# Kernel tuning notes

Measured on AMD Instinct MI355X. Metric: run time of the kernel, lower is better.

Reference implementation:

```python
import jax, jax.numpy as jnp
import numpy as np

D = 768
HID = 4 * D
B = 16
HRES = 32
WRES = 32
T = HRES * WRES


def layernorm(x, g, b, eps=1e-5):
    m = jnp.mean(x, axis=-1, keepdims=True)
    v = jnp.mean(jnp.square(x - m), axis=-1, keepdims=True)
    return (x - m) * jax.lax.rsqrt(v + eps) * g + b


def q_shift(x, H, W):
    # Vision-RWKV quad-directional token shift: split channels into 4 groups,
    # each group takes the neighboring patch's value in one direction (zero pad).
    Bn, N, C = x.shape
    xi = x.reshape(Bn, H, W, C)
    c = C // 4
    g0 = jnp.pad(xi[:, :, :-1, 0 * c:1 * c], ((0, 0), (0, 0), (1, 0), (0, 0)))  # from left
    g1 = jnp.pad(xi[:, :, 1:, 1 * c:2 * c], ((0, 0), (0, 0), (0, 1), (0, 0)))   # from right
    g2 = jnp.pad(xi[:, :-1, :, 2 * c:3 * c], ((0, 0), (1, 0), (0, 0), (0, 0)))  # from above
    g3 = jnp.pad(xi[:, 1:, :, 3 * c:4 * c], ((0, 0), (0, 1), (0, 0), (0, 0)))   # from below
    return jnp.concatenate([g0, g1, g2, g3], axis=-1).reshape(Bn, N, C)


def wkv_scan(w_log, u, k, v):
    # Numerically stable RWKV WKV recurrence (per-channel linear attention).
    # k, v: [B, T, C]; w = -exp(w_log) is the per-channel decay, u the bonus.
    w = -jnp.exp(w_log)
    kT = jnp.swapaxes(k, 0, 1)  # [T, B, C]
    vT = jnp.swapaxes(v, 0, 1)
    Bn, C = k.shape[0], k.shape[2]
    aa0 = jnp.zeros((Bn, C), k.dtype)
    bb0 = jnp.zeros((Bn, C), k.dtype)
    pp0 = jnp.full((Bn, C), -1e30, k.dtype)

    def step(carry, kv):
        aa, bb, pp = carry
        kt, vt = kv
        ww = u + kt
        p = jnp.maximum(pp, ww)
        e1 = jnp.exp(pp - p)
        e2 = jnp.exp(ww - p)
        out = (e1 * aa + e2 * vt) / (e1 * bb + e2)
        ww2 = pp + w
        p2 = jnp.maximum(ww2, kt)
        e1b = jnp.exp(ww2 - p2)
        e2b = jnp.exp(kt - p2)
        return (e1b * aa + e2b * vt, e1b * bb + e2b, p2), out

    _, outT = jax.lax.scan(step, (aa0, bb0, pp0), (kT, vT))
    return jnp.swapaxes(outT, 0, 1)  # [B, T, C]


def setup_inputs() -> dict:
    key = jax.random.key(0)
    ks = jax.random.split(key, 16)

    def nrm(k, shape, s=0.02):
        return jax.random.normal(k, shape, jnp.float32) * s

    return {
        "x": jax.random.normal(ks[0], (B, T, D), jnp.float32),
        "H": HRES,
        "W": WRES,
        "ln1_g": jnp.ones((D,), jnp.float32),
        "ln1_b": jnp.zeros((D,), jnp.float32),
        "ln2_g": jnp.ones((D,), jnp.float32),
        "ln2_b": jnp.zeros((D,), jnp.float32),
        "mu_k": jax.random.uniform(ks[1], (D,), jnp.float32),
        "mu_v": jax.random.uniform(ks[2], (D,), jnp.float32),
        "mu_r": jax.random.uniform(ks[3], (D,), jnp.float32),
        "w_log": nrm(ks[4], (D,), 0.5),
        "u": nrm(ks[5], (D,), 0.5),
        "Wk": nrm(ks[6], (D, D)),
        "Wv": nrm(ks[7], (D, D)),
        "Wr": nrm(ks[8], (D, D)),
        "Wo": nrm(ks[9], (D, D)),
        "cmu_k": jax.random.uniform(ks[10], (D,), jnp.float32),
        "cmu_r": jax.random.uniform(ks[11], (D,), jnp.float32),
        "Ck": nrm(ks[12], (HID, D)),
        "Cv": nrm(ks[13], (D, HID)),
        "Cr": nrm(ks[14], (D, D)),
    }


def reference(x, H, W, ln1_g, ln1_b, ln2_g, ln2_b, mu_k, mu_v, mu_r, w_log, u,
              Wk, Wv, Wr, Wo, cmu_k, cmu_r, Ck, Cv, Cr):
    h = x
    # ---- spatial mix (RWKV time-mix over patch sequence) ----
    a = layernorm(h, ln1_g, ln1_b)
    sx = q_shift(a, H, W)
    xk = a * mu_k + sx * (1.0 - mu_k)
    xv = a * mu_v + sx * (1.0 - mu_v)
    xr = a * mu_r + sx * (1.0 - mu_r)
    k = xk @ Wk.T
    v = xv @ Wv.T
    r = jax.nn.sigmoid(xr @ Wr.T)
    wkv = wkv_scan(w_log, u, k, v)
    h = h + (r * wkv) @ Wo.T
    # ---- channel mix (squared-ReLU gated FFN) ----
    a2 = layernorm(h, ln2_g, ln2_b)
    sx2 = q_shift(a2, H, W)
    xk2 = a2 * cmu_k + sx2 * (1.0 - cmu_k)
    xr2 = a2 * cmu_r + sx2 * (1.0 - cmu_r)
    kk = jnp.square(jax.nn.relu(xk2 @ Ck.T))
    h = h + jax.nn.sigmoid(xr2 @ Cr.T) * (kk @ Cv.T)
    # ---- outer residual from RWKVBlock.forward ----
    return h + x
```

## Files before the change

### kernel.cpp

```cpp
#include <hip/hip_runtime.h>
#include <hip/hip_bf16.h>

#define DD   768
#define TT   1024
#define BBATCH 16
#define NROWS (BBATCH * TT)
#define HIDN 3072
#define HHALF 1536
#define HH 32
#define WW 32
#define DW  (DD * DD)
#define DH  (DD * HIDN)
#define CCH 64
#define PCH (TT / CCH)

typedef float  floatx4 __attribute__((ext_vector_type(4)));
typedef __bf16 bf16x8  __attribute__((ext_vector_type(8)));

__device__ __forceinline__ float bf2f(__hip_bfloat16 v) { return __bfloat162float(v); }
__device__ __forceinline__ __hip_bfloat16 f2bf(float v) { return __float2bfloat16(v); }
__device__ __forceinline__ float toF(__hip_bfloat16 v) { return __bfloat162float(v); }
__device__ __forceinline__ float toF(float v) { return v; }

__device__ __forceinline__ void load4f(const float* __restrict__ p, float o[4]) {
    const float4 v = *reinterpret_cast<const float4*>(p);
    o[0] = v.x; o[1] = v.y; o[2] = v.z; o[3] = v.w;
}
__device__ __forceinline__ void load4f(const __hip_bfloat16* __restrict__ p, float o[4]) {
    const ushort4 v = *reinterpret_cast<const ushort4*>(p);
    o[0] = bf2f(__hip_bfloat16_raw{v.x});
    o[1] = bf2f(__hip_bfloat16_raw{v.y});
    o[2] = bf2f(__hip_bfloat16_raw{v.z});
    o[3] = bf2f(__hip_bfloat16_raw{v.w});
}
__device__ __forceinline__ void load8f(const float* __restrict__ p, float o[8]) {
    load4f(p, o); load4f(p + 4, o + 4);
}
__device__ __forceinline__ void load8f(const __hip_bfloat16* __restrict__ p, float o[8]) {
    const uint4 v = *reinterpret_cast<const uint4*>(p);
    const unsigned short* s = reinterpret_cast<const unsigned short*>(&v);
#pragma unroll
    for (int e = 0; e < 8; ++e) o[e] = bf2f(__hip_bfloat16_raw{s[e]});
}

#define GL2LDS(gp, lp)  __builtin_amdgcn_global_load_lds(                     \
    (const __attribute__((address_space(1))) void*)(gp),                      \
    (__attribute__((address_space(3))) void*)(lp), 16, 0, 0)

__global__ __launch_bounds__(256)
void cvt_all(const float* __restrict__ w0, const float* __restrict__ w1,
             const float* __restrict__ w2, const float* __restrict__ w3,
             const float* __restrict__ w4, const float* __restrict__ w5,
             const float* __restrict__ w6, __hip_bfloat16* __restrict__ dst)
{
    const int b = blockIdx.x;
    const float* s; size_t dofs; int rel;
    if (b < 2880) {
        const int seg = b / 576; rel = b - seg * 576;
        s = seg == 0 ? w0 : seg == 1 ? w1 : seg == 2 ? w2 : seg == 3 ? w3 : w4;
        dofs = (size_t)seg * DW;
    } else if (b < 5184) {
        rel = b - 2880; s = w5; dofs = 5ull * DW;
    } else {
        rel = b - 5184; s = w6; dofs = 5ull * DW + DH;
    }
    const int i = rel * 1024 + threadIdx.x * 4;
    const float4 v = *reinterpret_cast<const float4*>(s + i);
    __hip_bfloat16 o[4] = {f2bf(v.x), f2bf(v.y), f2bf(v.z), f2bf(v.w)};
    *reinterpret_cast<ushort4*>(&dst[dofs + i]) = *reinterpret_cast<const ushort4*>(o);
}

template <typename TIN>
__global__ __launch_bounds__(256)
void ln_stats_k(const TIN* __restrict__ x,
                float* __restrict__ mean, float* __restrict__ rstd)
{
    const int row  = blockIdx.x * 4 + (threadIdx.x >> 6);
    const int lane = threadIdx.x & 63;
    const TIN* xr = x + (size_t)row * DD;
    float s1 = 0.f, s2 = 0.f;
#pragma unroll
    for (int q = 0; q < 3; ++q) {
        float v4[4];
        load4f(xr + 4 * lane + 256 * q, v4);
#pragma unroll
        for (int e = 0; e < 4; ++e) { s1 += v4[e]; s2 += v4[e] * v4[e]; }
    }
#pragma unroll
    for (int off = 32; off > 0; off >>= 1) {
        s1 += __shfl_down(s1, off);
        s2 += __shfl_down(s2, off);
    }
    if (lane == 0) {
        const float m = s1 * (1.f / DD);
        mean[row] = m;
        rstd[row] = rsqrtf(s2 * (1.f / DD) - m * m + 1e-5f);
    }
}

template <typename TIN, int NOUT>
__global__ __launch_bounds__(256)
void mix_k(const TIN* __restrict__ x,
           const float* __restrict__ mean, const float* __restrict__ rstd,
           const float* __restrict__ g, const float* __restrict__ b,
           const float* __restrict__ muk,
           const float* __restrict__ muv,
           const float* __restrict__ mur,
           __hip_bfloat16* __restrict__ xk,
           __hip_bfloat16* __restrict__ xv,
           __hip_bfloat16* __restrict__ xr)
{
    const size_t i8 = ((size_t)blockIdx.x * 256 + threadIdx.x) * 8;
    const int c  = (int)(i8 % DD);
    const int n  = (int)((i8 / DD) % TT);
    const int bb = (int)(i8 / ((size_t)DD * TT));
    const int y = n >> 5, xp = n & 31;
    const int grow = bb * TT + n;

    const int grp = c / (DD / 4);
    int ny = y, nx = xp; bool ok;
    if      (grp == 0) { nx = xp - 1; ok = xp > 0;      }
    else if (grp == 1) { nx = xp + 1; ok = xp < WW - 1; }
    else if (grp == 2) { ny = y - 1;  ok = y > 0;       }
    else               { ny = y + 1;  ok = y < HH - 1;  }

    float gg[8], bbv[8];
    load8f(g + c, gg); load8f(b + c, bbv);

    float xc[8];
    load8f(x + (size_t)grow * DD + c, xc);
    const float m = mean[grow], rs = rstd[grow];
    float av[8], sx[8] = {0.f, 0.f, 0.f, 0.f, 0.f, 0.f, 0.f, 0.f};
#pragma unroll
    for (int e = 0; e < 8; ++e) av[e] = (xc[e] - m) * rs * gg[e] + bbv[e];

    if (ok) {
        const int nrow = bb * TT + ny * WW + nx;
        float xn[8];
        load8f(x + (size_t)nrow * DD + c, xn);
        const float m2 = mean[nrow], rs2 = rstd[nrow];
#pragma unroll
        for (int e = 0; e < 8; ++e) sx[e] = (xn[e] - m2) * rs2 * gg[e] + bbv[e];
    }

    float mk[8], mr[8];
    load8f(muk + c, mk); load8f(mur + c, mr);
    __hip_bfloat16 ok8[8], or8[8];
#pragma unroll
    for (int e = 0; e < 8; ++e) {
        ok8[e] = f2bf(av[e] * mk[e] + sx[e] * (1.f - mk[e]));
        or8[e] = f2bf(av[e] * mr[e] + sx[e] * (1.f - mr[e]));
    }
    *reinterpret_cast<uint4*>(&xk[i8]) = *reinterpret_cast<const uint4*>(ok8);
    *reinterpret_cast<uint4*>(&xr[i8]) = *reinterpret_cast<const uint4*>(or8);
    if (NOUT == 3) {
        float mv[8];
        load8f(muv + c, mv);
        __hip_bfloat16 ov8[8];
#pragma unroll
        for (int e = 0; e < 8; ++e)
            ov8[e] = f2bf(av[e] * mv[e] + sx[e] * (1.f - mv[e]));
        *reinterpret_cast<uint4*>(&xv[i8]) = *reinterpret_cast<const uint4*>(ov8);
    }
}

__device__ __forceinline__ void xpose_band(const floatx4 accRow[4], float* scr,
                                           int lane, float cv[16])
{
    const int l15 = lane & 15, quad = lane >> 4;
#pragma unroll
    for (int j = 0; j < 4; ++j)
#pragma unroll
        for (int r = 0; r < 4; ++r)
            scr[(quad * 4 + r) * 68 + j * 16 + l15] = accRow[j][r];
    const int row_l = lane >> 2, cb = (lane & 3) * 16;
#pragma unroll
    for (int q = 0; q < 4; ++q)
        *reinterpret_cast<float4*>(&cv[q * 4]) =
            *reinterpret_cast<const float4*>(&scr[row_l * 68 + cb + q * 4]);
}

template <int MODE>
__device__ __forceinline__ void mode_store(
    const float cv[16], size_t idx,
    __hip_bfloat16* __restrict__ outB, float* __restrict__ outF,
    const __hip_bfloat16* __restrict__ auxS, const __hip_bfloat16* __restrict__ auxH,
    const float* __restrict__ auxX, const float* __restrict__ auxG)
{
    if (MODE == 1 || MODE == 3) {
        __hip_bfloat16 ob[16];
#pragma unroll
        for (int e = 0; e < 16; ++e) {
            float v = cv[e];
            if (MODE == 1) v = 1.f / (1.f + __expf(-v));
            else { v = fmaxf(v, 0.f); v = v * v; }
            ob[e] = f2bf(v);
        }
        *reinterpret_cast<uint4*>(&outB[idx])     = *reinterpret_cast<const uint4*>(&ob[0]);
        *reinterpret_cast<uint4*>(&outB[idx + 8]) = *reinterpret_cast<const uint4*>(&ob[8]);
    } else if (MODE == 2) {
        float xv[16];
#pragma unroll
        for (int q = 0; q < 4; ++q)
            *reinterpret_cast<float4*>(&xv[q * 4]) =
                *reinterpret_cast<const float4*>(&auxX[idx + q * 4]);
        __hip_bfloat16 ob[16];
#pragma unroll
        for (int e = 0; e < 16; ++e) ob[e] = f2bf(cv[e] + xv[e]);
        *reinterpret_cast<uint4*>(&outB[idx])     = *reinterpret_cast<const uint4*>(&ob[0]);
        *reinterpret_cast<uint4*>(&outB[idx + 8]) = *reinterpret_cast<const uint4*>(&ob[8]);
    } else if (MODE == 4) {
        unsigned short hs[16], ss[16]; float xv[16], ov[16];
        *reinterpret_cast<uint4*>(&hs[0]) = *reinterpret_cast<const uint4*>(&auxH[idx]);
        *reinterpret_cast<uint4*>(&hs[8]) = *reinterpret_cast<const uint4*>(&auxH[idx + 8]);
        *reinterpret_cast<uint4*>(&ss[0]) = *reinterpret_cast<const uint4*>(&auxS[idx]);
        *reinterpret_cast<uint4*>(&ss[8]) = *reinterpret_cast<const uint4*>(&auxS[idx + 8]);
#pragma unroll
        for (int q = 0; q < 4; ++q)
            *reinterpret_cast<float4*>(&xv[q * 4]) =
                *reinterpret_cast<const float4*>(&auxX[idx + q * 4]);
#pragma unroll
        for (int e = 0; e < 16; ++e)
            ov[e] = bf2f(__hip_bfloat16_raw{hs[e]})
                  + bf2f(__hip_bfloat16_raw{ss[e]}) * cv[e] + xv[e];
#pragma unroll
        for (int q = 0; q < 4; ++q)
            *reinterpret_cast<float4*>(&outF[idx + q * 4]) =
                *reinterpret_cast<const float4*>(&ov[q * 4]);
    } else if (MODE == 5) {
        unsigned short ss[16]; float ov[16];
        *reinterpret_cast<uint4*>(&ss[0]) = *reinterpret_cast<const uint4*>(&auxS[idx]);
        *reinterpret_cast<uint4*>(&ss[8]) = *reinterpret_cast<const uint4*>(&auxS[idx + 8]);
#pragma unroll
        for (int q = 0; q < 4; ++q)
            *reinterpret_cast<float4*>(&ov[q * 4]) =
                *reinterpret_cast<const float4*>(&outF[idx + q * 4]);
#pragma unroll
        for (int e = 0; e < 16; ++e)
            ov[e] += bf2f(__hip_bfloat16_raw{ss[e]}) * cv[e];
#pragma unroll
        for (int q = 0; q < 4; ++q)
            *reinterpret_cast<float4*>(&outF[idx + q * 4]) =
                *reinterpret_cast<const float4*>(&ov[q * 4]);
    } else if (MODE == 6) {
        unsigned short hs[16]; float xv[16], gf[16], ov[16];
        *reinterpret_cast<uint4*>(&hs[0]) = *reinterpret_cast<const uint4*>(&auxH[idx]);
        *reinterpret_cast<uint4*>(&hs[8]) = *reinterpret_cast<const uint4*>(&auxH[idx + 8]);
#pragma unroll
        for (int q = 0; q < 4; ++q) {
            *reinterpret_cast<float4*>(&xv[q * 4]) =
                *reinterpret_cast<const float4*>(&auxX[idx + q * 4]);
            *reinterpret_cast<float4*>(&gf[q * 4]) =
                *reinterpret_cast<const float4*>(&auxG[idx + q * 4]);
        }
#pragma unroll
        for (int e = 0; e < 16; ++e)
            ov[e] = bf2f(__hip_bfloat16_raw{hs[e]}) + gf[e] * cv[e] + xv[e];
#pragma unroll
        for (int q = 0; q < 4; ++q)
            *reinterpret_cast<float4*>(&outF[idx + q * 4]) =
                *reinterpret_cast<const float4*>(&ov[q * 4]);
    } else {
        float ov[16];
#pragma unroll
        for (int e = 0; e < 16; ++e)
            ov[e] = 1.f / (1.f + __expf(-cv[e]));
#pragma unroll
        for (int q = 0; q < 4; ++q)
            *reinterpret_cast<float4*>(&outF[idx + q * 4]) =
                *reinterpret_cast<const float4*>(&ov[q * 4]);
    }
}

#define BM 128
#define BN 128
#define BKK 64

__device__ __forceinline__ void gemm_core(
    const __hip_bfloat16* __restrict__ A, const __hip_bfloat16* __restrict__ W,
    int K, int Wstr, int bm, int bn, unsigned short* lds, floatx4 acc[4][4])
{
    const int tid  = threadIdx.x;
    const int lane = tid & 63, wid = tid >> 6;
    const int l15  = lane & 15, quad = lane >> 4;
    const int m0   = (wid & 1) * 64;
    const int n0   = (wid >> 1) * 64;
    const int srow  = lane >> 3;
    const int gcolg = (lane & 7) ^ srow;
    const int s0    = wid * 4;
    const int swzbase = l15 & 7;

    for (int k0 = 0; k0 < K; k0 += BKK) {
#pragma unroll
        for (int t = 0; t < 4; ++t) {
            const int s   = s0 + t;
            const int row = s * 8 + srow;
            GL2LDS(A + (size_t)(bm * BM + row) * K    + k0 + gcolg * 8,
                   &lds[s * 512]);
            GL2LDS(W + (size_t)(bn * BN + row) * Wstr + k0 + gcolg * 8,
                   &lds[8192 + s * 512]);
        }
        __syncthreads();
#pragma unroll
        for (int kk = 0; kk < BKK; kk += 32) {
            const int swz = (((kk >> 3) + quad) ^ swzbase) * 8;
            bf16x8 afr[4], bfr[4];
#pragma unroll
            for (int i = 0; i < 4; ++i)
                afr[i] = *reinterpret_cast<const bf16x8*>(
                    &lds[(m0 + i * 16 + l15) * BKK + swz]);
#pragma unroll
            for (int j = 0; j < 4; ++j)
                bfr[j] = *reinterpret_cast<const bf16x8*>(
                    &lds[8192 + (n0 + j * 16 + l15) * BKK + swz]);
#pragma unroll
            for (int i = 0; i < 4; ++i)
#pragma unroll
                for (int j = 0; j < 4; ++j)
                    acc[i][j] = __builtin_amdgcn_mfma_f32_16x16x32_bf16(
                        afr[i], bfr[j], acc[i][j], 0, 0, 0);
        }
        __syncthreads();
    }
}

template <int MODE>
__global__ __launch_bounds__(256, 2)
void gemm_bt(const __hip_bfloat16* __restrict__ A,
             const __hip_bfloat16* __restrict__ W,
             int K, int Wstr, int Nn,
             __hip_bfloat16* __restrict__ outB,
             float* __restrict__ outF,
             const __hip_bfloat16* __restrict__ auxS,
             const __hip_bfloat16* __restrict__ auxH,
             const float* __restrict__ auxX,
             const float* __restrict__ auxG)
{
    __shared__ __align__(16) unsigned short lds[16384];
    const int bm = blockIdx.x, bn = blockIdx.y;
    const int tid = threadIdx.x, lane = tid & 63, wid = tid >> 6;
    const int m0 = (wid & 1) * 64, n0 = (wid >> 1) * 64;

    floatx4 acc[4][4];
#pragma unroll
    for (int i = 0; i < 4; ++i)
#pragma unroll
        for (int j = 0; j < 4; ++j)
            acc[i][j] = floatx4{0.f, 0.f, 0.f, 0.f};

    gemm_core(A, W, K, Wstr, bm, bn, lds, acc);

    float* scr = reinterpret_cast<float*>(lds) + wid * 1088;
    const int row_l = lane >> 2, cb = (lane & 3) * 16;
#pragma unroll
    for (int i = 0; i < 4; ++i) {
        float cv[16];
        xpose_band(acc[i], scr, lane, cv);
        const int grow = bm * BM + m0 + i * 16 + row_l;
        const int gcol = bn * BN + n0 + cb;
        const size_t idx = (size_t)grow * Nn + gcol;
        mode_store<MODE>(cv, idx, outB, outF, auxS, auxH, auxX, auxG);
    }
}

__global__ __launch_bounds__(256, 2)
void gemm_qkv(const __hip_bfloat16* __restrict__ A0, const __hip_bfloat16* __restrict__ A1,
              const __hip_bfloat16* __restrict__ A2,
              const __hip_bfloat16* __restrict__ W0, const __hip_bfloat16* __restrict__ W1,
              const __hip_bfloat16* __restrict__ W2,
              __hip_bfloat16* __restrict__ O0, __hip_bfloat16* __restrict__ O1,
              __hip_bfloat16* __restrict__ O2)
{
    __shared__ __align__(16) unsigned short lds[16384];
    const int z = blockIdx.z;
    const __hip_bfloat16* A = z == 0 ? A0 : z == 1 ? A1 : A2;
    const __hip_bfloat16* W = z == 0 ? W0 : z == 1 ? W1 : W2;
    __hip_bfloat16*       O = z == 0 ? O0 : z == 1 ? O1 : O2;
    const int bm = blockIdx.x, bn = blockIdx.y;
    const int tid = threadIdx.x, lane = tid & 63, wid = tid >> 6;
    const int m0 = (wid & 1) * 64, n0 = (wid >> 1) * 64;

    floatx4 acc[4][4];
#pragma unroll
    for (int i = 0; i < 4; ++i)
#pragma unroll
        for (int j = 0; j < 4; ++j)
            acc[i][j] = floatx4{0.f, 0.f, 0.f, 0.f};

    gemm_core(A, W, DD, DD, bm, bn, lds, acc);

    float* scr = reinterpret_cast<float*>(lds) + wid * 1088;
    const int row_l = lane >> 2, cb = (lane & 3) * 16;
#pragma unroll
    for (int i = 0; i < 4; ++i) {
        float cv[16];
        xpose_band(acc[i], scr, lane, cv);
        const int grow = bm * BM + m0 + i * 16 + row_l;
        const int gcol = bn * BN + n0 + cb;
        const size_t idx = (size_t)grow * DD + gcol;
        __hip_bfloat16 ob[16];
#pragma unroll
        for (int e = 0; e < 16; ++e) {
            float v = cv[e];
            if (z == 2) v = 1.f / (1.f + __expf(-v));
            ob[e] = f2bf(v);
        }
        *reinterpret_cast<uint4*>(&O[idx])     = *reinterpret_cast<const uint4*>(&ob[0]);
        *reinterpret_cast<uint4*>(&O[idx + 8]) = *reinterpret_cast<const uint4*>(&ob[8]);
    }
}

__global__ __launch_bounds__(192)
void wkv_passA(const float* __restrict__ w_log,
               const __hip_bfloat16* __restrict__ k,
               const __hip_bfloat16* __restrict__ v,
               float* __restrict__ SA, float* __restrict__ SB,
               float* __restrict__ SP)
{
    const int c  = threadIdx.x * 4;
    const int j  = blockIdx.x;
    const int bb = blockIdx.y;
    float wl[4];
    load4f(w_log + c, wl);
    const float w4[4] = {-__expf(wl[0]), -__expf(wl[1]), -__expf(wl[2]), -__expf(wl[3])};
    const size_t base = ((size_t)bb * TT + j * CCH) * DD + c;
    float a[4] = {0.f, 0.f, 0.f, 0.f}, b2[4] = {0.f, 0.f, 0.f, 0.f};
    float p[4] = {-1e30f, -1e30f, -1e30f, -1e30f};
#pragma unroll 4
    for (int t = 0; t < CCH; ++t) {
        const size_t o = base + (size_t)t * DD;
        float kt[4], vt[4];
        load4f(k + o, kt);
        load4f(v + o, vt);
#pragma unroll
        for (int e = 0; e < 4; ++e) {
            const float ww2 = p[e] + w4[e];
            const float p2  = fmaxf(ww2, kt[e]);
            const float e1  = __expf(ww2 - p2);
            const float e2  = __expf(kt[e] - p2);
            a[e]  = e1 * a[e]  + e2 * vt[e];
            b2[e] = e1 * b2[e] + e2;
            p[e]  = p2;
        }
    }
    const size_t si = ((size_t)bb * PCH + j) * DD + c;
    *reinterpret_cast<float4*>(&SA[si]) = float4{a[0], a[1], a[2], a[3]};
    *reinterpret_cast<float4*>(&SB[si]) = float4{b2[0], b2[1], b2[2], b2[3]};
    *reinterpret_cast<float4*>(&SP[si]) = float4{p[0], p[1], p[2], p[3]};
}

__global__ __launch_bounds__(256)
void wkv_scanj(const float* __restrict__ w_log,
               float* __restrict__ SA, float* __restrict__ SB,
               float* __restrict__ SP)
{
    const int idx = blockIdx.x * 256 + threadIdx.x;
    const int c = (idx * 4) % DD, bb = (idx * 4) / DD;
    float wl[4];
    load4f(w_log + c, wl);
    float wC[4];
#pragma unroll
    for (int e = 0; e < 4; ++e) wC[e] = -__expf(wl[e]) * (float)CCH;
    float a[4] = {0.f, 0.f, 0.f, 0.f}, b2[4] = {0.f, 0.f, 0.f, 0.f};
    float p[4] = {-1e30f, -1e30f, -1e30f, -1e30f};
#pragma unroll
    for (int j = 0; j < PCH; ++j) {
        const size_t si = ((size_t)bb * PCH + j) * DD + c;
        float aj[4], bj[4], pj[4];
        load4f(SA + si, aj); load4f(SB + si, bj); load4f(SP + si, pj);
        *reinterpret_cast<float4*>(&SA[si]) = float4{a[0], a[1], a[2], a[3]};
        *reinterpret_cast<float4*>(&SB[si]) = float4{b2[0], b2[1], b2[2], b2[3]};
        *reinterpret_cast<float4*>(&SP[si]) = float4{p[0], p[1], p[2], p[3]};
#pragma unroll
        for (int e = 0; e < 4; ++e) {
            const float pd = p[e] + wC[e];
            const float pn = fmaxf(pd, pj[e]);
            const float e1 = __expf(pd - pn);
            const float e2 = __expf(pj[e] - pn);
            a[e]  = e1 * a[e]  + e2 * aj[e];
            b2[e] = e1 * b2[e] + e2 * bj[e];
            p[e]  = pn;
        }
    }
}

__global__ __launch_bounds__(192)
void wkv_passB(const float* __restrict__ w_log, const float* __restrict__ u,
               const __hip_bfloat16* __restrict__ k,
               const __hip_bfloat16* __restrict__ v,
               const __hip_bfloat16* __restrict__ r,
               __hip_bfloat16* __restrict__ rw,
               const float* __restrict__ SA, const float* __restrict__ SB,
               const float* __restrict__ SP)
{
    const int c  = threadIdx.x * 4;
    const int j  = blockIdx.x;
    const int bb = blockIdx.y;
    float wl[4], uu[4];
    load4f(w_log + c, wl);
    load4f(u + c, uu);
    const float w4[4] = {-__expf(wl[0]), -__expf(wl[1]), -__expf(wl[2]), -__expf(wl[3])};
    const size_t si = ((size_t)bb * PCH + j) * DD + c;
    float aa[4], bbv[4], pp[4];
    load4f(SA + si, aa); load4f(SB + si, bbv); load4f(SP + si, pp);
    const size_t base = ((size_t)bb * TT + j * CCH) * DD + c;
#pragma unroll 4
    for (int t = 0; t < CCH; ++t) {
        const size_t o = base + (size_t)t * DD;
        float kt[4], vt[4], rt[4];
        load4f(k + o, kt);
        load4f(v + o, vt);
        load4f(r + o, rt);
        __hip_bfloat16 ob[4];
#pragma unroll
        for (int e = 0; e < 4; ++e) {
            const float ww = uu[e] + kt[e];
            const float pm = fmaxf(pp[e], ww);
            const float e1 = __expf(pp[e] - pm);
            const float e2 = __expf(ww - pm);
            const float ov = __fdividef(e1 * aa[e] + e2 * vt[e], e1 * bbv[e] + e2);
            ob[e] = f2bf(rt[e] * ov);
            const float ww2 = pp[e] + w4[e];
            const float p2  = fmaxf(ww2, kt[e]);
            const float e1b = __expf(ww2 - p2);
            const float e2b = __expf(kt[e] - p2);
            aa[e]  = e1b * aa[e]  + e2b * vt[e];
            bbv[e] = e1b * bbv[e] + e2b;
            pp[e]  = p2;
        }
        *reinterpret_cast<ushort4*>(&rw[o]) = *reinterpret_cast<const ushort4*>(ob);
    }
}

extern "C" void kernel_launch(void* const* d_in, const int* in_sizes, int n_in,
                              void* d_out, int out_size, void* d_ws, size_t ws_size,
                              hipStream_t stream)
{
    (void)in_sizes; (void)n_in; (void)out_size;
    const float* x     = (const float*)d_in[0];
    const float* ln1_g = (const float*)d_in[3];
    const float* ln1_b = (const float*)d_in[4];
    const float* ln2_g = (const float*)d_in[5];
    const float* ln2_b = (const float*)d_in[6];
    const float* mu_k  = (const float*)d_in[7];
    const float* mu_v  = (const float*)d_in[8];
    const float* mu_r  = (const float*)d_in[9];
    const float* w_log = (const float*)d_in[10];
    const float* u     = (const float*)d_in[11];
    const float* Wk    = (const float*)d_in[12];
    const float* Wv    = (const float*)d_in[13];
    const float* Wr    = (const float*)d_in[14];
    const float* Wo    = (const float*)d_in[15];
    const float* cmu_k = (const float*)d_in[16];
    const float* cmu_r = (const float*)d_in[17];
    const float* Ck    = (const float*)d_in[18];
    const float* Cv    = (const float*)d_in[19];
    const float* Cr    = (const float*)d_in[20];
    float* out = (float*)d_out;

    const size_t ND = (size_t)NROWS * DD;
    const size_t SL = ND * 2;
    const size_t WBYTES = (size_t)(5 * DW + 2 * DH) * 2;
    const size_t NSTATE = (size_t)BBATCH * PCH * DD;
    const size_t TAIL = WBYTES + 2 * (size_t)NROWS * sizeof(float)
                      + 3 * NSTATE * sizeof(float);
    int nslots;
    if      (ws_size >= 7 * SL + TAIL) nslots = 7;
    else if (ws_size >= 6 * SL + TAIL) nslots = 6;
    else if (ws_size >= 5 * SL + TAIL) nslots = 5;
    else return;

    char* w = (char*)d_ws;
    __hip_bfloat16* S0 = (__hip_bfloat16*)(w);
    __hip_bfloat16* S1 = (__hip_bfloat16*)(w + 1 * SL);
    __hip_bfloat16* S2 = (__hip_bfloat16*)(w + 2 * SL);
    __hip_bfloat16* S3 = (__hip_bfloat16*)(w + 3 * SL);
    __hip_bfloat16* S4 = (__hip_bfloat16*)(w + 4 * SL);
    __hip_bfloat16* S5 = (__hip_bfloat16*)(w + 5 * SL);
    __hip_bfloat16* WB  = (__hip_bfloat16*)(w + (size_t)nslots * SL);
    __hip_bfloat16* WkB = WB;
    __hip_bfloat16* WvB = WB + 1ull * DW;
    __hip_bfloat16* WrB = WB + 2ull * DW;
    __hip_bfloat16* WoB = WB + 3ull * DW;
    __hip_bfloat16* CrB = WB + 4ull * DW;
    __hip_bfloat16* CkB = WB + 5ull * DW;
    __hip_bfloat16* CvB = CkB + DH;
    float* meanB = (float*)(w + (size_t)nslots * SL + WBYTES);
    float* rstdB = meanB + NROWS;
    float* SAb = rstdB + NROWS;
    float* SBb = SAb + NSTATE;
    float* SPb = SBb + NSTATE;

    const int LN_GRID  = NROWS / 4;
    const int MIX_GRID = (int)(ND / 2048);
    const dim3 g768(NROWS / BM, DD / BN);
    const dim3 g1536(NROWS / BM, HHALF / BN);
    const dim3 gCk(NROWS / BM, HIDN / BN);
    const dim3 gqkv3(NROWS / BM, DD / BN, 3);
    const dim3 gqkv2(NROWS / BM, DD / BN, 2);
    const dim3 gwkv(PCH, BBATCH);
    const int SCANJ_GRID = (BBATCH * DD / 4) / 256;

    cvt_all<<<7488, 256, 0, stream>>>(Wk, Wv, Wr, Wo, Cr, Ck, Cv, WB);

    ln_stats_k<float><<<LN_GRID, 256, 0, stream>>>(x, meanB, rstdB);
    mix_k<float, 3><<<MIX_GRID, 256, 0, stream>>>(x, meanB, rstdB, ln1_g, ln1_b,
                                                  mu_k, mu_v, mu_r, S0, S1, S2);

    if (nslots == 7) {
        gemm_qkv<<<gqkv3, 256, 0, stream>>>(S0, S1, S2, WkB, WvB, WrB, S3, S4, S5);
        wkv_passA<<<gwkv, 192, 0, stream>>>(w_log, S3, S4, SAb, SBb, SPb);
        wkv_scanj<<<SCANJ_GRID, 256, 0, stream>>>(w_log, SAb, SBb, SPb);
        wkv_passB<<<gwkv, 192, 0, stream>>>(w_log, u, S3, S4, S5, S1, SAb, SBb, SPb);
        gemm_bt<2><<<g768, 256, 0, stream>>>(S1, WoB, DD, DD, DD, S2, nullptr,
                                             nullptr, nullptr, x, nullptr);
        ln_stats_k<__hip_bfloat16><<<LN_GRID, 256, 0, stream>>>(S2, meanB, rstdB);
        mix_k<__hip_bfloat16, 2><<<MIX_GRID, 256, 0, stream>>>(S2, meanB, rstdB, ln2_g, ln2_b,
                                                               cmu_k, nullptr, cmu_r,
                                                               S0, nullptr, S3);
        gemm_bt<1><<<g768, 256, 0, stream>>>(S3, CrB, DD, DD, DD, S1, nullptr,
                                             nullptr, nullptr, nullptr, nullptr);
        gemm_bt<3><<<gCk, 256, 0, stream>>>(S0, CkB, DD, DD, HIDN,
                                            S3, nullptr, nullptr, nullptr, nullptr, nullptr);
        gemm_bt<4><<<g768, 256, 0, stream>>>(S3, CvB, HIDN, HIDN, DD,
                                             nullptr, out, S1, S2, x, nullptr);
    } else if (nslots == 6) {
        gemm_qkv<<<gqkv3, 256, 0, stream>>>(S0, S1, S2, WkB, WvB, WrB, S3, S4, S5);
        wkv_passA<<<gwkv, 192, 0, stream>>>(w_log, S3, S4, SAb, SBb, SPb);
        wkv_scanj<<<SCANJ_GRID, 256, 0, stream>>>(w_log, SAb, SBb, SPb);
        wkv_passB<<<gwkv, 192, 0, stream>>>(w_log, u, S3, S4, S5, S0, SAb, SBb, SPb);
        gemm_bt<2><<<g768, 256, 0, stream>>>(S0, WoB, DD, DD, DD, S1, nullptr,
                                             nullptr, nullptr, x, nullptr);
        ln_stats_k<__hip_bfloat16><<<LN_GRID, 256, 0, stream>>>(S1, meanB, rstdB);
        mix_k<__hip_bfloat16, 2><<<MIX_GRID, 256, 0, stream>>>(S1, meanB, rstdB, ln2_g, ln2_b,
                                                               cmu_k, nullptr, cmu_r,
                                                               S0, nullptr, S2);
        gemm_bt<7><<<g768, 256, 0, stream>>>(S2, CrB, DD, DD, DD, nullptr, out,
                                             nullptr, nullptr, nullptr, nullptr);
        gemm_bt<3><<<gCk, 256, 0, stream>>>(S0, CkB, DD, DD, HIDN,
                                            S2, nullptr, nullptr, nullptr, nullptr, nullptr);
        gemm_bt<6><<<g768, 256, 0, stream>>>(S2, CvB, HIDN, HIDN, DD,
                                             nullptr, out, nullptr, S1, x, out);
    } else {
        gemm_qkv<<<gqkv2, 256, 0, stream>>>(S0, S1, nullptr, WkB, WvB, nullptr,
                                            S3, S4, nullptr);
        gemm_bt<1><<<g768, 256, 0, stream>>>(S2, WrB, DD, DD, DD, S0, nullptr,
                                             nullptr, nullptr, nullptr, nullptr);
        wkv_passA<<<gwkv, 192, 0, stream>>>(w_log, S3, S4, SAb, SBb, SPb);
        wkv_scanj<<<SCANJ_GRID, 256, 0, stream>>>(w_log, SAb, SBb, SPb);
        wkv_passB<<<gwkv, 192, 0, stream>>>(w_log, u, S3, S4, S0, S1, SAb, SBb, SPb);
        gemm_bt<2><<<g768, 256, 0, stream>>>(S1, WoB, DD, DD, DD, S2, nullptr,
                                             nullptr, nullptr, x, nullptr);
        ln_stats_k<__hip_bfloat16><<<LN_GRID, 256, 0, stream>>>(S2, meanB, rstdB);
        mix_k<__hip_bfloat16, 2><<<MIX_GRID, 256, 0, stream>>>(S2, meanB, rstdB, ln2_g, ln2_b,
                                                               cmu_k, nullptr, cmu_r,
                                                               S0, nullptr, S3);
        gemm_bt<1><<<g768, 256, 0, stream>>>(S3, CrB, DD, DD, DD, S1, nullptr,
                                             nullptr, nullptr, nullptr, nullptr);
        __hip_bfloat16* kk = S3;
        gemm_bt<3><<<g1536, 256, 0, stream>>>(S0, CkB, DD, DD, HHALF,
                                              kk, nullptr, nullptr, nullptr, nullptr, nullptr);
        gemm_bt<4><<<g768, 256, 0, stream>>>(kk, CvB, HHALF, HIDN, DD,
                                             nullptr, out, S1, S2, x, nullptr);
        gemm_bt<3><<<g1536, 256, 0, stream>>>(S0, CkB + (size_t)HHALF * DD, DD, DD, HHALF,
                                              kk, nullptr, nullptr, nullptr, nullptr, nullptr);
        gemm_bt<5><<<g768, 256, 0, stream>>>(kk, CvB + HHALF, HHALF, HIDN, DD,
                                             nullptr, out, S1, nullptr, nullptr, nullptr);
    }
}
```

Baseline: 540.5 us.

## Add 256x256-tile 8-wave pipelined GEMM for channel-mix Ck and Cv

Adds a new GEMM kernel with 256x256 output tiles, 512 threads and double-buffered global-to-LDS async loads interleaved with MFMA quarters under barriers and raised wave priority. It also adds a swizzled block-to-tile mapping. The kernel replaces the 128x128 GEMM for the two large channel-mix matmuls (Ck expansion and Cv projection). The goal is more operand reuse per loaded byte and better overlap of loads with MFMA. The cost is heavy register and LDS use (128KB LDS per block), fewer blocks per CU, and a possible wave-quantization tail on the smaller 768-wide grid.

```diff
diff --git a/kernel.cpp b/kernel.cpp
--- a/kernel.cpp
+++ b/kernel.cpp
@@ -47,6 +47,12 @@
     (const __attribute__((address_space(1))) void*)(gp),                      \
     (__attribute__((address_space(3))) void*)(lp), 16, 0, 0)
 
+#define BARX() __builtin_amdgcn_s_barrier()
+#define WAITV6() do { asm volatile("s_waitcnt vmcnt(6)");                      \
+    __builtin_amdgcn_sched_barrier(0); } while (0)
+#define WAITV0() do { asm volatile("s_waitcnt vmcnt(0)");                      \
+    __builtin_amdgcn_sched_barrier(0); } while (0)
+
 __global__ __launch_bounds__(256)
 void cvt_all(const float* __restrict__ w0, const float* __restrict__ w1,
              const float* __restrict__ w2, const float* __restrict__ w3,
@@ -269,6 +275,143 @@
         for (int q = 0; q < 4; ++q)
             *reinterpret_cast<float4*>(&outF[idx + q * 4]) =
                 *reinterpret_cast<const float4*>(&ov[q * 4]);
+    }
+}
+
+#define STG256(tau, j)                                                         \
+  do { if ((tau) * 64 < K) {                                                   \
+    const int _sb = ((((tau) & 1) * 4) + (j)) * 8192;                          \
+    const int _k0 = (tau) * 64;                                                \
+    const __hip_bfloat16 *_s0, *_s1;                                           \
+    if ((j) < 2) {                                                             \
+      _s0 = A + (size_t)(bmr + (j) * 128 + r0) * K + _k0 + colg;               \
+      _s1 = A + (size_t)(bmr + (j) * 128 + r1) * K + _k0 + colg;               \
+    } else {                                                                   \
+      const int _w0 = bnr + ((j) == 2 ? 128 : 0);                              \
+      _s0 = W + (size_t)(_w0 + r0) * Wstr + _k0 + colg;                        \
+      _s1 = W + (size_t)(_w0 + r1) * Wstr + _k0 + colg;                        \
+    }                                                                          \
+    GL2LDS(_s0, &lds[_sb + wid * 512]);                                        \
+    GL2LDS(_s1, &lds[_sb + 4096 + wid * 512]);                                 \
+  } } while (0)
+
+#define LDA_H(buf, mh)                                                         \
+  { const int _ab = ((buf) * 4 + wr) * 8192;                                   \
+    _Pragma("unroll") for (int mf = 0; mf < 4; ++mf)                           \
+    _Pragma("unroll") for (int k2 = 0; k2 < 2; ++k2)                           \
+      af[(mh) * 4 + mf][k2] = *reinterpret_cast<const bf16x8*>(                \
+        &lds[_ab + (((mh) * 4 + mf) * 16 + l15) * 64                           \
+             + (((k2 * 4 + quad) ^ sw7) * 8)]); }
+
+#define LDB_TO(dst, buf, nh)                                                   \
+  { const int _bb = ((buf) * 4 + ((wc >> 1) ? 2 : 3)) * 8192;                  \
+    _Pragma("unroll") for (int nf = 0; nf < 2; ++nf)                           \
+    _Pragma("unroll") for (int k2 = 0; k2 < 2; ++k2)                           \
+      dst[nf][k2] = *reinterpret_cast<const bf16x8*>(                          \
+        &lds[_bb + ((wc & 1) * 64 + (nh) * 32 + nf * 16 + l15) * 64            \
+             + (((k2 * 4 + quad) ^ sw7) * 8)]); }
+
+#define MFQ(MH, NH, BARR)                                                      \
+  _Pragma("unroll") for (int mf = 0; mf < 4; ++mf)                             \
+  _Pragma("unroll") for (int nf = 0; nf < 2; ++nf)                             \
+  _Pragma("unroll") for (int k2 = 0; k2 < 2; ++k2)                             \
+    acc[(MH) * 4 + mf][(NH) * 2 + nf] =                                        \
+      __builtin_amdgcn_mfma_f32_16x16x32_bf16(af[(MH) * 4 + mf][k2],           \
+        BARR[nf][k2], acc[(MH) * 4 + mf][(NH) * 2 + nf], 0, 0, 0);
+
+#define TILE_STEP(tt, buf)                                                     \
+  {                                                                            \
+    LDA_H(buf, 0); LDB_TO(bfa, buf, 0);                                        \
+    STG256((tt) + 1, 3);                                                       \
+    BARX();                                                                    \
+    __builtin_amdgcn_s_setprio(1); MFQ(0, 0, bfa); __builtin_amdgcn_s_setprio(0);\
+    BARX();                                                                    \
+    LDA_H(buf, 1);                                                             \
+    BARX();                                                                    \
+    __builtin_amdgcn_s_setprio(1); MFQ(1, 0, bfa); __builtin_amdgcn_s_setprio(0);\
+    BARX();                                                                    \
+    LDB_TO(bfb, buf, 1);                                                       \
+    STG256((tt) + 2, 0);                                                       \
+    BARX();                                                                    \
+    __builtin_amdgcn_s_setprio(1); MFQ(0, 1, bfb); __builtin_amdgcn_s_setprio(0);\
+    BARX();                                                                    \
+    STG256((tt) + 2, 1);                                                       \
+    STG256((tt) + 2, 2);                                                       \
+    BARX();                                                                    \
+    __builtin_amdgcn_s_setprio(1); MFQ(1, 1, bfb); __builtin_amdgcn_s_setprio(0);\
+    if ((tt) + 2 == nt) { WAITV0(); } else { WAITV6(); }                       \
+    BARX();                                                                    \
+  }
+
+struct G256Ctx {
+    int bm, bn;
+    int tid, lane, wid, wr, wc, l15, quad, sw7, r0, r1, colg;
+};
+
+__device__ __forceinline__ void g256_decode(G256Ctx& c, int b, int nbn, int nwg)
+{
+    const int s = (b & 7) * (nwg >> 3) + (b >> 3);
+    c.bm = s / nbn; c.bn = s % nbn;
+    c.tid = threadIdx.x; c.lane = c.tid & 63; c.wid = c.tid >> 6;
+    c.wr = c.wid >> 2; c.wc = c.wid & 3;
+    c.l15 = c.lane & 15; c.quad = c.lane >> 4; c.sw7 = c.l15 & 7;
+    c.r0 = c.tid >> 3; c.r1 = c.r0 + 64;
+    c.colg = ((c.tid & 7) ^ (c.r0 & 7)) * 8;
+}
+
+__device__ __forceinline__ void g256_core(
+    const __hip_bfloat16* __restrict__ A, const __hip_bfloat16* __restrict__ W,
+    int K, int Wstr, const G256Ctx& c, unsigned short* lds, floatx4 acc[8][4])
+{
+    const int bmr = c.bm * 256, bnr = c.bn * 256;
+    const int wid = c.wid, wr = c.wr, wc = c.wc;
+    const int l15 = c.l15, quad = c.quad, sw7 = c.sw7;
+    const int r0 = c.r0, r1 = c.r1, colg = c.colg;
+    const int nt = K >> 6;
+
+    bf16x8 af[8][2], bfa[2][2], bfb[2][2];
+
+    STG256(0, 0); STG256(0, 1); STG256(0, 2); STG256(0, 3);
+    STG256(1, 0); STG256(1, 1); STG256(1, 2);
+    WAITV6();
+    BARX();
+
+    for (int t = 0; t < nt; t += 2) {
+        TILE_STEP(t, 0);
+        TILE_STEP(t + 1, 1);
+    }
+    WAITV0();
+}
+
+template <int MODE>
+__global__ __launch_bounds__(512, 2)
+void gemm256(const __hip_bfloat16* __restrict__ A, const __hip_bfloat16* __restrict__ W,
+             int K, int Wstr, int Nn,
+             __hip_bfloat16* __restrict__ outB, float* __restrict__ outF,
+             const __hip_bfloat16* __restrict__ auxS, const __hip_bfloat16* __restrict__ auxH,
+             const float* __restrict__ auxX, const float* __restrict__ auxG)
+{
+    __shared__ __align__(16) unsigned short lds[65536];
+    G256Ctx c; g256_decode(c, blockIdx.x, Nn >> 8, gridDim.x);
+
+    floatx4 acc[8][4];
+#pragma unroll
+    for (int i = 0; i < 8; ++i)
+#pragma unroll
+        for (int j = 0; j < 4; ++j) acc[i][j] = floatx4{0.f, 0.f, 0.f, 0.f};
+
+    g256_core(A, W, K, Wstr, c, lds, acc);
+
+    float* scr = reinterpret_cast<float*>(lds) + c.wid * 1088;
+    const int row_l = c.lane >> 2, cb = (c.lane & 3) * 16;
+#pragma unroll
+    for (int i = 0; i < 8; ++i) {
+        float cv[16];
+        xpose_band(acc[i], scr, c.lane, cv);
+        const int grow = c.bm * 256 + c.wr * 128 + i * 16 + row_l;
+        const int gcol = c.bn * 256 + c.wc * 64 + cb;
+        const size_t idx = (size_t)grow * Nn + gcol;
+        mode_store<MODE>(cv, idx, outB, outF, auxS, auxH, auxX, auxG);
     }
 }
 
@@ -595,11 +738,12 @@
     const int MIX_GRID = (int)(ND / 2048);
     const dim3 g768(NROWS / BM, DD / BN);
     const dim3 g1536(NROWS / BM, HHALF / BN);
-    const dim3 gCk(NROWS / BM, HIDN / BN);
     const dim3 gqkv3(NROWS / BM, DD / BN, 3);
     const dim3 gqkv2(NROWS / BM, DD / BN, 2);
     const dim3 gwkv(PCH, BBATCH);
     const int SCANJ_GRID = (BBATCH * DD / 4) / 256;
+    const int G256_768 = (NROWS / 256) * (DD / 256);
+    const int G256_HID = (NROWS / 256) * (HIDN / 256);
 
     cvt_all<<<7488, 256, 0, stream>>>(Wk, Wv, Wr, Wo, Cr, Ck, Cv, WB);
 
@@ -620,10 +764,10 @@
                                                                S0, nullptr, S3);
         gemm_bt<1><<<g768, 256, 0, stream>>>(S3, CrB, DD, DD, DD, S1, nullptr,
                                              nullptr, nullptr, nullptr, nullptr);
-        gemm_bt<3><<<gCk, 256, 0, stream>>>(S0, CkB, DD, DD, HIDN,
-                                            S3, nullptr, nullptr, nullptr, nullptr, nullptr);
-        gemm_bt<4><<<g768, 256, 0, stream>>>(S3, CvB, HIDN, HIDN, DD,
-                                             nullptr, out, S1, S2, x, nullptr);
+        gemm256<3><<<G256_HID, 512, 0, stream>>>(S0, CkB, DD, DD, HIDN,
+                                                 S3, nullptr, nullptr, nullptr, nullptr, nullptr);
+        gemm256<4><<<G256_768, 512, 0, stream>>>(S3, CvB, HIDN, HIDN, DD,
+                                                 nullptr, out, S1, S2, x, nullptr);
     } else if (nslots == 6) {
         gemm_qkv<<<gqkv3, 256, 0, stream>>>(S0, S1, S2, WkB, WvB, WrB, S3, S4, S5);
         wkv_passA<<<gwkv, 192, 0, stream>>>(w_log, S3, S4, SAb, SBb, SPb);
@@ -637,10 +781,10 @@
                                                                S0, nullptr, S2);
         gemm_bt<7><<<g768, 256, 0, stream>>>(S2, CrB, DD, DD, DD, nullptr, out,
                                              nullptr, nullptr, nullptr, nullptr);
-        gemm_bt<3><<<gCk, 256, 0, stream>>>(S0, CkB, DD, DD, HIDN,
-                                            S2, nullptr, nullptr, nullptr, nullptr, nullptr);
-        gemm_bt<6><<<g768, 256, 0, stream>>>(S2, CvB, HIDN, HIDN, DD,
-                                             nullptr, out, nullptr, S1, x, out);
+        gemm256<3><<<G256_HID, 512, 0, stream>>>(S0, CkB, DD, DD, HIDN,
+                                                 S2, nullptr, nullptr, nullptr, nullptr, nullptr);
+        gemm256<6><<<G256_768, 512, 0, stream>>>(S2, CvB, HIDN, HIDN, DD,
+                                                 nullptr, out, nullptr, S1, x, out);
     } else {
         gemm_qkv<<<gqkv2, 256, 0, stream>>>(S0, S1, nullptr, WkB, WvB, nullptr,
                                             S3, S4, nullptr);
```

Result: slower. 627.5 us (+16.1%).
